# Kernel optimization log

Hardware: AMD Instinct MI355X
Metric: run time of the kernel (lower is better)

The kernel has to match this reference:

```python
import jax, jax.numpy as jnp
import numpy as np

N_INPUT, N_HIDDEN, N_OUTPUT = 64, 1024, 64
B, T = 128, 512

def setup_inputs() -> dict:
    key = jax.random.key(0)
    ks = jax.random.split(key, 8)
    s_in = 1.0 / np.sqrt(N_INPUT)
    s_h = 1.0 / np.sqrt(N_HIDDEN)
    return {
        "x": jax.random.normal(ks[0], (B, T, N_INPUT), jnp.float32),
        "enc_w": jax.random.uniform(ks[1], (N_HIDDEN, N_INPUT), jnp.float32, -s_in, s_in),
        "enc_b": jax.random.uniform(ks[2], (N_HIDDEN,), jnp.float32, -s_in, s_in),
        "rec_w": jax.random.uniform(ks[3], (N_HIDDEN, N_HIDDEN), jnp.float32, -s_h, s_h),
        "fgt_w": jax.random.uniform(ks[4], (N_HIDDEN, N_HIDDEN), jnp.float32, -s_h, s_h),
        "dec_w": jax.random.uniform(ks[5], (N_OUTPUT, N_HIDDEN), jnp.float32, -s_h, s_h),
        "dec_b": jax.random.uniform(ks[6], (N_OUTPUT,), jnp.float32, -s_h, s_h),
        "hinit_w": jax.random.uniform(ks[7], (N_HIDDEN, 1), jnp.float32, -1.0, 1.0),
        "hinit_b": jax.random.uniform(jax.random.fold_in(key, 9), (N_HIDDEN,), jnp.float32, -1.0, 1.0),
    }

def softsign(x):
    return x / (1.0 + jnp.abs(x))

def reference(x, enc_w, enc_b, rec_w, fgt_w, dec_w, dec_b, hinit_w, hinit_b):
    # x: [B, T, I] -> time-major [T, B, I]
    xt = jnp.transpose(x, (1, 0, 2))
    # hidden_init(ones(B,1)) = ones @ hinit_w^T + b = broadcast of column sum
    hidden0 = jnp.broadcast_to(hinit_w[:, 0] + hinit_b, (x.shape[0], hinit_b.shape[0]))
    # Precompute encoder projection for all timesteps (same math, one big GEMM)
    enc_all = jnp.einsum('tbi,hi->tbh', xt, enc_w) + enc_b  # [T, B, H]

    def step(hidden, enc_t):
        forget = jax.nn.sigmoid(hidden @ fgt_w.T)
        hidden_new = softsign(enc_t + hidden @ rec_w.T)
        hidden = (1.0 - forget) * hidden + forget * hidden_new
        out_t = hidden @ dec_w.T + dec_b
        return hidden, out_t

    hidden, output = jax.lax.scan(step, hidden0, enc_all)
    return output, hidden  # output: [T, B, O], hidden: [B, H]
```

## Files before the change

kernel.cpp:

```cpp
#include <hip/hip_runtime.h>

typedef unsigned short u16;

#define NWG 256
#define NT  256
#define TS  512
#define HD  1024
#define BS  128
#define NI  64
#define NO  64
#define XR  16
#define CC  32
#define RCP 17

typedef __attribute__((ext_vector_type(8))) short bf16x8;
typedef __attribute__((ext_vector_type(4))) float f32x4;

__device__ __forceinline__ float bf2f(u16 u) {
    union { unsigned int i; float f; } v; v.i = ((unsigned int)u) << 16; return v.f;
}
__device__ __forceinline__ u16 f2bf(float f) {
    union { float fl; unsigned int i; } v; v.fl = f;
    unsigned int x = v.i;
    return (u16)((x + 0x7fffu + ((x >> 16) & 1u)) >> 16);
}
__device__ __forceinline__ float ldv(const void* p, size_t i, bool isf32) {
    return isf32 ? ((const float*)p)[i] : bf2f(((const u16*)p)[i]);
}

__device__ __forceinline__ unsigned l2_atomic_add(unsigned* p, unsigned v) {
    unsigned old;
    asm volatile("global_atomic_add %0, %1, %2, off sc0\n\t"
                 "s_waitcnt vmcnt(0)"
                 : "=&v"(old) : "v"(p), "v"(v) : "memory");
    return old;
}
__device__ __forceinline__ void l2_atomic_swap_nr(unsigned* p, unsigned v) {
    asm volatile("global_atomic_swap %0, %1, off" :: "v"(p), "v"(v) : "memory");
}

__device__ __forceinline__ void load_a_frags(const u16* ap, bf16x8* a) {
    asm volatile(
        "global_load_dwordx4 %0, %8, off sc0\n\t"
        "global_load_dwordx4 %1, %8, off offset:64 sc0\n\t"
        "global_load_dwordx4 %2, %8, off offset:128 sc0\n\t"
        "global_load_dwordx4 %3, %8, off offset:192 sc0\n\t"
        "global_load_dwordx4 %4, %8, off offset:256 sc0\n\t"
        "global_load_dwordx4 %5, %8, off offset:320 sc0\n\t"
        "global_load_dwordx4 %6, %8, off offset:384 sc0\n\t"
        "global_load_dwordx4 %7, %8, off offset:448 sc0\n\t"
        "s_waitcnt vmcnt(0)"
        : "=&v"(a[0]), "=&v"(a[1]), "=&v"(a[2]), "=&v"(a[3]),
          "=&v"(a[4]), "=&v"(a[5]), "=&v"(a[6]), "=&v"(a[7])
        : "v"(ap) : "memory");
}

#define MBL 16

__global__ __launch_bounds__(NT)
void arnn_xcd(const void* __restrict__ xv,
              const void* __restrict__ encwv,
              const void* __restrict__ encbv,
              const void* __restrict__ recwv,
              const void* __restrict__ fgtwv,
              const void* __restrict__ decwv,
              const void* __restrict__ decbv,
              const void* __restrict__ hinitwv,
              const void* __restrict__ hinitbv,
              void* __restrict__ outv,
              u16* __restrict__ h0buf,
              u16* __restrict__ h1buf,
              unsigned* __restrict__ tickets,
              unsigned* __restrict__ mboxes)
{
    __shared__ short WB[132 * 64 * 8];
    __shared__ float redC[4 * 5 * 16 * RCP];
    __shared__ unsigned s_xcd, s_slot;
    __shared__ int s_f32;

    const int tid  = threadIdx.x;
    const int wave = tid >> 6;
    const int lane = tid & 63;
    const int m    = lane & 15;
    const int quad = lane >> 4;

    if (tid == 0) {
        unsigned xcc;
        asm volatile("s_getreg_b32 %0, hwreg(HW_REG_XCC_ID, 0, 4)" : "=s"(xcc));
        xcc &= 7u;
        unsigned slot = l2_atomic_add(tickets + xcc * 16, 1u);
        s_xcd = xcc;
        s_slot = slot & 31u;
        s_f32 = 0;
    }
    __syncthreads();
    {
        float v = bf2f(((const u16*)recwv)[tid]);
        if (!(v >= -1.0f && v <= 1.0f)) s_f32 = 1;
    }
    __syncthreads();
    const bool isf32 = (s_f32 != 0);
    const int xcd  = (int)s_xcd;
    const int slot = (int)s_slot;
    const int b0   = xcd * XR;
    const int j0   = slot * CC;
    const int dt   = slot & 3;
    unsigned* mbX   = mboxes + (size_t)xcd * 32 * 4 * MBL;
    unsigned* mbW   = mbX + (slot * 4 + wave) * MBL;
    const int pw = (slot >> 3), pi = (slot & 7);

    for (int idx = tid; idx < 132 * 64; idx += NT) {
        int ksg = idx >> 6, l = idx & 63, n = l & 15, q = l >> 4;
        int tile, ksl;
        if (ksg < 34)       { tile = 0; ksl = ksg; }
        else if (ksg < 68)  { tile = 1; ksl = ksg - 34; }
        else if (ksg < 100) { tile = 2; ksl = ksg - 68; }
        else                { tile = 3; ksl = ksg - 100; }
        int j = j0 + ((tile & 1) << 4) + n;
        bf16x8 v;
        if (!isf32) {
            const u16* src;
            if (tile < 2) src = (ksl < 32) ? (const u16*)recwv + (size_t)j * HD + ksl * 32 + q * 8
                                           : (const u16*)encwv + (size_t)j * NI + (ksl - 32) * 32 + q * 8;
            else          src = (const u16*)fgtwv + (size_t)j * HD + ksl * 32 + q * 8;
            v = *(const bf16x8*)src;
        } else {
            const float* src;
            if (tile < 2) src = (ksl < 32) ? (const float*)recwv + (size_t)j * HD + ksl * 32 + q * 8
                                           : (const float*)encwv + (size_t)j * NI + (ksl - 32) * 32 + q * 8;
            else          src = (const float*)fgtwv + (size_t)j * HD + ksl * 32 + q * 8;
            #pragma unroll
            for (int i = 0; i < 8; ++i) v[i] = (short)f2bf(src[i]);
        }
        *(bf16x8*)&WB[idx * 8] = v;
    }
    __syncthreads();

    bf16x8 Breg[2][8];
    bf16x8 Freg[2][8];
    #pragma unroll
    for (int ks = 0; ks < 8; ++ks) {
        int kb = wave * 8 + ks;
        Breg[0][ks] = *(const bf16x8*)&WB[((0   + kb) * 64 + lane) * 8];
        Breg[1][ks] = *(const bf16x8*)&WB[((34  + kb) * 64 + lane) * 8];
        Freg[0][ks] = *(const bf16x8*)&WB[((68  + kb) * 64 + lane) * 8];
        Freg[1][ks] = *(const bf16x8*)&WB[((100 + kb) * 64 + lane) * 8];
    }
    bf16x8 Ereg[2];
    if (wave < 2) {
        Ereg[0] = *(const bf16x8*)&WB[((32 + wave) * 64 + lane) * 8];
        Ereg[1] = *(const bf16x8*)&WB[((34 + 32 + wave) * 64 + lane) * 8];
    }
    bf16x8 dfr[8];
    {
        int o = 16 * dt + m;
        #pragma unroll
        for (int ks = 0; ks < 8; ++ks) {
            int kb = wave * 256 + ks * 32 + quad * 8;
            if (!isf32) dfr[ks] = *(const bf16x8*)((const u16*)decwv + (size_t)o * HD + kb);
            else {
                const float* src = (const float*)decwv + (size_t)o * HD + kb;
                #pragma unroll
                for (int i = 0; i < 8; ++i) dfr[ks][i] = (short)f2bf(src[i]);
            }
        }
    }
    const int er = tid >> 5, ec = tid & 31;
    float encb_r = ldv(encbv, j0 + ec, isf32);
    float decb_r = ldv(decbv, 16 * dt + (tid & 15), isf32);
    float h0v = ldv(hinitwv, j0 + ec, isf32) + ldv(hinitbv, j0 + ec, isf32);
    float hstA = h0v, hstB = h0v;
    h0buf[(size_t)(b0 + er    ) * HD + j0 + ec] = f2bf(h0v);
    h0buf[(size_t)(b0 + er + 8) * HD + j0 + ec] = f2bf(h0v);
    __syncthreads();
    if (tid < 32)
        l2_atomic_swap_nr(mbX + (tid * 4 + pw) * MBL + pi, 1u);

    for (int t = 0; t < TS; ++t) {
        f32x4 acc[5];
        #pragma unroll
        for (int tt = 0; tt < 5; ++tt) acc[tt] = (f32x4){0.f, 0.f, 0.f, 0.f};

        if (wave < 2) {
            bf16x8 xf;
            size_t xb = (size_t)(b0 + m) * (TS * NI) + (size_t)t * NI + wave * 32 + quad * 8;
            if (!isf32) xf = *(const bf16x8*)((const u16*)xv + xb);
            else {
                const float* xp = (const float*)xv + xb;
                #pragma unroll
                for (int i = 0; i < 8; ++i) xf[i] = (short)f2bf(xp[i]);
            }
            acc[0] = __builtin_amdgcn_mfma_f32_16x16x32_bf16(xf, Ereg[0], acc[0], 0, 0, 0);
            acc[1] = __builtin_amdgcn_mfma_f32_16x16x32_bf16(xf, Ereg[1], acc[1], 0, 0, 0);
        }

        {
            const unsigned target = (unsigned)(t + 1);
            for (;;) {
                unsigned v = target;
                if (lane < 8) v = l2_atomic_add(mbW + lane, 0u);
                if (__all((int)(v >= target))) break;
            }
        }

        const u16* cur = (t & 1) ? h1buf : h0buf;
        u16*       nxt = (t & 1) ? h0buf : h1buf;

        bf16x8 a[8];
        load_a_frags(cur + (size_t)(b0 + m) * HD + wave * 256 + quad * 8, a);

        #pragma unroll
        for (int ks = 0; ks < 8; ++ks) {
            acc[0] = __builtin_amdgcn_mfma_f32_16x16x32_bf16(a[ks], Breg[0][ks], acc[0], 0, 0, 0);
            acc[1] = __builtin_amdgcn_mfma_f32_16x16x32_bf16(a[ks], Breg[1][ks], acc[1], 0, 0, 0);
            acc[2] = __builtin_amdgcn_mfma_f32_16x16x32_bf16(a[ks], Freg[0][ks], acc[2], 0, 0, 0);
            acc[3] = __builtin_amdgcn_mfma_f32_16x16x32_bf16(a[ks], Freg[1][ks], acc[3], 0, 0, 0);
            acc[4] = __builtin_amdgcn_mfma_f32_16x16x32_bf16(a[ks], dfr[ks],     acc[4], 0, 0, 0);
        }

        #pragma unroll
        for (int tt = 0; tt < 5; ++tt) {
            #pragma unroll
            for (int r = 0; r < 4; ++r)
                redC[((wave * 5 + tt) * 16 + quad * 4 + r) * RCP + m] = acc[tt][r];
        }
        __syncthreads();

        {
            const int tl = ec >> 4, col = ec & 15;
            float pr0 = encb_r, pf0 = 0.f, pr1 = encb_r, pf1 = 0.f;
            #pragma unroll
            for (int kq = 0; kq < 4; ++kq) {
                pr0 += redC[((kq * 5 + tl) * 16 + er) * RCP + col];
                pf0 += redC[((kq * 5 + 2 + tl) * 16 + er) * RCP + col];
                pr1 += redC[((kq * 5 + tl) * 16 + er + 8) * RCP + col];
                pf1 += redC[((kq * 5 + 2 + tl) * 16 + er + 8) * RCP + col];
            }
            float fg0 = 1.0f / (1.0f + __expf(-pf0));
            float hn0 = pr0 / (1.0f + fabsf(pr0));
            hstA = hstA + fg0 * (hn0 - hstA);
            nxt[(size_t)(b0 + er) * HD + j0 + ec] = f2bf(hstA);
            float fg1 = 1.0f / (1.0f + __expf(-pf1));
            float hn1 = pr1 / (1.0f + fabsf(pr1));
            hstB = hstB + fg1 * (hn1 - hstB);
            nxt[(size_t)(b0 + er + 8) * HD + j0 + ec] = f2bf(hstB);
        }
        if (slot < 4 && t > 0) {
            int r = tid >> 4, col = tid & 15;
            float o = decb_r;
            #pragma unroll
            for (int kq = 0; kq < 4; ++kq)
                o += redC[((kq * 5 + 4) * 16 + r) * RCP + col];
            size_t oi = (size_t)(t - 1) * (BS * NO) + (size_t)(b0 + r) * NO + 16 * dt + col;
            if (isf32) ((float*)outv)[oi] = o; else ((u16*)outv)[oi] = f2bf(o);
        }
        __syncthreads();
        if (tid < 32)
            l2_atomic_swap_nr(mbX + (tid * 4 + pw) * MBL + pi, (unsigned)(t + 2));
    }

    if (slot < 4) {
        {
            const unsigned target = (unsigned)(TS + 1);
            for (;;) {
                unsigned v = target;
                if (lane < 8) v = l2_atomic_add(mbW + lane, 0u);
                if (__all((int)(v >= target))) break;
            }
        }
        bf16x8 a[8];
        load_a_frags(h0buf + (size_t)(b0 + m) * HD + wave * 256 + quad * 8, a);
        f32x4 ac = (f32x4){0.f, 0.f, 0.f, 0.f};
        #pragma unroll
        for (int ks = 0; ks < 8; ++ks)
            ac = __builtin_amdgcn_mfma_f32_16x16x32_bf16(a[ks], dfr[ks], ac, 0, 0, 0);
        #pragma unroll
        for (int r = 0; r < 4; ++r)
            redC[((wave * 5 + 4) * 16 + quad * 4 + r) * RCP + m] = ac[r];
        __syncthreads();
        {
            int r = tid >> 4, col = tid & 15;
            float o = decb_r;
            #pragma unroll
            for (int kq = 0; kq < 4; ++kq)
                o += redC[((kq * 5 + 4) * 16 + r) * RCP + col];
            size_t oi = (size_t)511 * (BS * NO) + (size_t)(b0 + r) * NO + 16 * dt + col;
            if (isf32) ((float*)outv)[oi] = o; else ((u16*)outv)[oi] = f2bf(o);
        }
    }
    {
        size_t oi0 = (size_t)TS * BS * NO + (size_t)(b0 + er) * HD + j0 + ec;
        size_t oi1 = (size_t)TS * BS * NO + (size_t)(b0 + er + 8) * HD + j0 + ec;
        if (isf32) { ((float*)outv)[oi0] = hstA; ((float*)outv)[oi1] = hstB; }
        else       { ((u16*)outv)[oi0] = f2bf(hstA); ((u16*)outv)[oi1] = f2bf(hstB); }
    }
}

extern "C" void kernel_launch(void* const* d_in, const int* in_sizes, int n_in,
                              void* d_out, int out_size, void* d_ws, size_t ws_size,
                              hipStream_t stream) {
    (void)in_sizes; (void)n_in; (void)out_size; (void)ws_size;
    const void* xv       = d_in[0];
    const void* encwv    = d_in[1];
    const void* encbv    = d_in[2];
    const void* recwv    = d_in[3];
    const void* fgtwv    = d_in[4];
    const void* decwv    = d_in[5];
    const void* decbv    = d_in[6];
    const void* hinitwv  = d_in[7];
    const void* hinitbv  = d_in[8];
    void* outv = d_out;

    unsigned* tickets = (unsigned*)d_ws;
    unsigned* mboxes  = (unsigned*)((char*)d_ws + 4096);
    u16* h0buf = (u16*)((char*)d_ws + 524288);
    u16* h1buf = h0buf + (size_t)BS * HD;

    hipMemsetAsync(d_ws, 0, 4096 + 8 * 32 * 4 * MBL * 4, stream);

    void* args[] = { (void*)&xv, (void*)&encwv, (void*)&encbv, (void*)&recwv,
                     (void*)&fgtwv, (void*)&decwv, (void*)&decbv,
                     (void*)&hinitwv, (void*)&hinitbv,
                     (void*)&outv, (void*)&h0buf, (void*)&h1buf,
                     (void*)&tickets, (void*)&mboxes };
    hipError_t err = hipLaunchCooperativeKernel((void*)arnn_xcd, dim3(NWG), dim3(NT), args, 0, stream);
    if (err != hipSuccess) {
        hipLaunchKernelGGL(arnn_xcd, dim3(NWG), dim3(NT), 0, stream,
                           xv, encwv, encbv, recwv, fgtwv, decwv, decbv,
                           hinitwv, hinitbv, outv, h0buf, h1buf, tickets, mboxes);
    }
}
```

Baseline: 1.410 ms.

## Prefetch next-step x, pack hidden writes, spread decoder output across all workgroups

Loads the next timestep's input slice during the current step's recurrent MFMA work, so the x load no longer sits on the per-step critical path. Each thread now owns two adjacent hidden columns of one row and writes them as a single packed 32-bit store instead of two scattered 16-bit stores. The decoder output reduction and store are split across all 32 slots, two rows each, instead of four slots doing sixteen rows. The output store now happens after the mailbox signal, taking it off the synchronisation path. This adds registers for the prefetched x and changes the redC read pattern.

```diff
diff --git a/kernel.cpp b/kernel.cpp
--- a/kernel.cpp
+++ b/kernel.cpp
@@ -105,6 +105,7 @@
     const int b0   = xcd * XR;
     const int j0   = slot * CC;
     const int dt   = slot & 3;
+    const int rg   = slot >> 2;
     unsigned* mbX   = mboxes + (size_t)xcd * 32 * 4 * MBL;
     unsigned* mbW   = mbX + (slot * 4 + wave) * MBL;
     const int pw = (slot >> 3), pi = (slot & 7);
@@ -165,17 +166,29 @@
             }
         }
     }
-    const int er = tid >> 5, ec = tid & 31;
-    float encb_r = ldv(encbv, j0 + ec, isf32);
+    const int er2 = tid >> 4, ec2 = (tid & 15) * 2;
+    float encb0 = ldv(encbv, j0 + ec2,     isf32);
+    float encb1 = ldv(encbv, j0 + ec2 + 1, isf32);
     float decb_r = ldv(decbv, 16 * dt + (tid & 15), isf32);
-    float h0v = ldv(hinitwv, j0 + ec, isf32) + ldv(hinitbv, j0 + ec, isf32);
-    float hstA = h0v, hstB = h0v;
-    h0buf[(size_t)(b0 + er    ) * HD + j0 + ec] = f2bf(h0v);
-    h0buf[(size_t)(b0 + er + 8) * HD + j0 + ec] = f2bf(h0v);
+    float hstA = ldv(hinitwv, j0 + ec2,     isf32) + ldv(hinitbv, j0 + ec2,     isf32);
+    float hstB = ldv(hinitwv, j0 + ec2 + 1, isf32) + ldv(hinitbv, j0 + ec2 + 1, isf32);
+    {
+        unsigned pack = (unsigned)f2bf(hstA) | ((unsigned)f2bf(hstB) << 16);
+        *(unsigned*)&h0buf[(size_t)(b0 + er2) * HD + j0 + ec2] = pack;
+    }
     __syncthreads();
     if (tid < 32)
         l2_atomic_swap_nr(mbX + (tid * 4 + pw) * MBL + pi, 1u);
 
+    bf16x8 xpB = {};
+    f32x4 xr0 = {}, xr1 = {};
+    if (wave < 2) {
+        size_t xb = (size_t)(b0 + m) * (TS * NI) + (size_t)0 * NI + wave * 32 + quad * 8;
+        if (!isf32) xpB = *(const bf16x8*)((const u16*)xv + xb);
+        else { const float* xp = (const float*)xv + xb;
+               xr0 = *(const f32x4*)xp; xr1 = *(const f32x4*)(xp + 4); }
+    }
+
     for (int t = 0; t < TS; ++t) {
         f32x4 acc[5];
         #pragma unroll
@@ -183,12 +196,13 @@
 
         if (wave < 2) {
             bf16x8 xf;
-            size_t xb = (size_t)(b0 + m) * (TS * NI) + (size_t)t * NI + wave * 32 + quad * 8;
-            if (!isf32) xf = *(const bf16x8*)((const u16*)xv + xb);
+            if (!isf32) xf = xpB;
             else {
-                const float* xp = (const float*)xv + xb;
                 #pragma unroll
-                for (int i = 0; i < 8; ++i) xf[i] = (short)f2bf(xp[i]);
+                for (int i = 0; i < 4; ++i) {
+                    xf[i]     = (short)f2bf(xr0[i]);
+                    xf[i + 4] = (short)f2bf(xr1[i]);
+                }
             }
             acc[0] = __builtin_amdgcn_mfma_f32_16x16x32_bf16(xf, Ereg[0], acc[0], 0, 0, 0);
             acc[1] = __builtin_amdgcn_mfma_f32_16x16x32_bf16(xf, Ereg[1], acc[1], 0, 0, 0);
@@ -209,6 +223,14 @@
         bf16x8 a[8];
         load_a_frags(cur + (size_t)(b0 + m) * HD + wave * 256 + quad * 8, a);
 
+        if (wave < 2) {
+            int tn = (t + 1 < TS) ? t + 1 : t;
+            size_t xb = (size_t)(b0 + m) * (TS * NI) + (size_t)tn * NI + wave * 32 + quad * 8;
+            if (!isf32) xpB = *(const bf16x8*)((const u16*)xv + xb);
+            else { const float* xp = (const float*)xv + xb;
+                   xr0 = *(const f32x4*)xp; xr1 = *(const f32x4*)(xp + 4); }
+        }
+
         #pragma unroll
         for (int ks = 0; ks < 8; ++ks) {
             acc[0] = __builtin_amdgcn_mfma_f32_16x16x32_bf16(a[ks], Breg[0][ks], acc[0], 0, 0, 0);
@@ -227,39 +249,44 @@
         __syncthreads();
 
         {
-            const int tl = ec >> 4, col = ec & 15;
-            float pr0 = encb_r, pf0 = 0.f, pr1 = encb_r, pf1 = 0.f;
+            const int tl = ec2 >> 4, c0 = ec2 & 15;
+            float pr0 = encb0, pf0 = 0.f, pr1 = encb1, pf1 = 0.f;
             #pragma unroll
             for (int kq = 0; kq < 4; ++kq) {
-                pr0 += redC[((kq * 5 + tl) * 16 + er) * RCP + col];
-                pf0 += redC[((kq * 5 + 2 + tl) * 16 + er) * RCP + col];
-                pr1 += redC[((kq * 5 + tl) * 16 + er + 8) * RCP + col];
-                pf1 += redC[((kq * 5 + 2 + tl) * 16 + er + 8) * RCP + col];
+                pr0 += redC[((kq * 5 + tl) * 16 + er2) * RCP + c0];
+                pf0 += redC[((kq * 5 + 2 + tl) * 16 + er2) * RCP + c0];
+                pr1 += redC[((kq * 5 + tl) * 16 + er2) * RCP + c0 + 1];
+                pf1 += redC[((kq * 5 + 2 + tl) * 16 + er2) * RCP + c0 + 1];
             }
             float fg0 = 1.0f / (1.0f + __expf(-pf0));
             float hn0 = pr0 / (1.0f + fabsf(pr0));
             hstA = hstA + fg0 * (hn0 - hstA);
-            nxt[(size_t)(b0 + er) * HD + j0 + ec] = f2bf(hstA);
             float fg1 = 1.0f / (1.0f + __expf(-pf1));
             float hn1 = pr1 / (1.0f + fabsf(pr1));
             hstB = hstB + fg1 * (hn1 - hstB);
-            nxt[(size_t)(b0 + er + 8) * HD + j0 + ec] = f2bf(hstB);
-        }
-        if (slot < 4 && t > 0) {
-            int r = tid >> 4, col = tid & 15;
-            float o = decb_r;
+            unsigned pack = (unsigned)f2bf(hstA) | ((unsigned)f2bf(hstB) << 16);
+            *(unsigned*)&nxt[(size_t)(b0 + er2) * HD + j0 + ec2] = pack;
+        }
+        float dec_o = 0.f;
+        int dr = 0;
+        if (tid < 32) {
+            dr = 2 * rg + (tid >> 4);
+            int col = tid & 15;
+            dec_o = decb_r;
             #pragma unroll
             for (int kq = 0; kq < 4; ++kq)
-                o += redC[((kq * 5 + 4) * 16 + r) * RCP + col];
-            size_t oi = (size_t)(t - 1) * (BS * NO) + (size_t)(b0 + r) * NO + 16 * dt + col;
-            if (isf32) ((float*)outv)[oi] = o; else ((u16*)outv)[oi] = f2bf(o);
+                dec_o += redC[((kq * 5 + 4) * 16 + dr) * RCP + col];
         }
         __syncthreads();
         if (tid < 32)
             l2_atomic_swap_nr(mbX + (tid * 4 + pw) * MBL + pi, (unsigned)(t + 2));
-    }
-
-    if (slot < 4) {
+        if (tid < 32 && t > 0) {
+            size_t oi = (size_t)(t - 1) * (BS * NO) + (size_t)(b0 + dr) * NO + 16 * dt + (tid & 15);
+            if (isf32) ((float*)outv)[oi] = dec_o; else ((u16*)outv)[oi] = f2bf(dec_o);
+        }
+    }
+
+    {
         {
             const unsigned target = (unsigned)(TS + 1);
             for (;;) {
@@ -278,21 +305,23 @@
         for (int r = 0; r < 4; ++r)
             redC[((wave * 5 + 4) * 16 + quad * 4 + r) * RCP + m] = ac[r];
         __syncthreads();
-        {
-            int r = tid >> 4, col = tid & 15;
+        if (tid < 32) {
+            int dr = 2 * rg + (tid >> 4), col = tid & 15;
             float o = decb_r;
             #pragma unroll
             for (int kq = 0; kq < 4; ++kq)
-                o += redC[((kq * 5 + 4) * 16 + r) * RCP + col];
-            size_t oi = (size_t)511 * (BS * NO) + (size_t)(b0 + r) * NO + 16 * dt + col;
+                o += redC[((kq * 5 + 4) * 16 + dr) * RCP + col];
+            size_t oi = (size_t)511 * (BS * NO) + (size_t)(b0 + dr) * NO + 16 * dt + col;
             if (isf32) ((float*)outv)[oi] = o; else ((u16*)outv)[oi] = f2bf(o);
         }
     }
     {
-        size_t oi0 = (size_t)TS * BS * NO + (size_t)(b0 + er) * HD + j0 + ec;
-        size_t oi1 = (size_t)TS * BS * NO + (size_t)(b0 + er + 8) * HD + j0 + ec;
-        if (isf32) { ((float*)outv)[oi0] = hstA; ((float*)outv)[oi1] = hstB; }
-        else       { ((u16*)outv)[oi0] = f2bf(hstA); ((u16*)outv)[oi1] = f2bf(hstB); }
+        size_t oi = (size_t)TS * BS * NO + (size_t)(b0 + er2) * HD + j0 + ec2;
+        if (isf32) { ((float*)outv)[oi] = hstA; ((float*)outv)[oi + 1] = hstB; }
+        else {
+            unsigned pack = (unsigned)f2bf(hstA) | ((unsigned)f2bf(hstB) << 16);
+            *(unsigned*)&((u16*)outv)[oi] = pack;
+        }
     }
 }
 
```

New measurement: 1.435 ms. About the same (+1.7%).
